# Kernel optimization log

Hardware: AMD Instinct MI355X
Metric: run time of the kernel (lower is better)

The kernel has to match this reference:

```python
import jax, jax.numpy as jnp
import numpy as np
from jax.scipy.linalg import expm

B, S, D, E, K, NROT = 2, 2048, 1024, 8, 2, 3
EPS = 1e-5


def setup_inputs() -> dict:
    key = jax.random.key(0)
    ks = jax.random.split(key, 16)
    sc = 0.02
    x = jax.random.normal(ks[0], (B, S, D), jnp.float32)
    ln_gamma = 1.0 + sc * jax.random.normal(ks[1], (D,), jnp.float32)
    ln_beta = sc * jax.random.normal(ks[2], (D,), jnp.float32)
    abel_w = sc * jax.random.normal(ks[3], (D, D), jnp.float32)
    abel_b = sc * jax.random.normal(ks[4], (D,), jnp.float32)
    moe_gate_w = sc * jax.random.normal(ks[5], (D, E), jnp.float32)
    moe_gate_b = sc * jax.random.normal(ks[6], (E,), jnp.float32)
    ew1 = sc * jax.random.normal(ks[7], (E, D, 2 * D), jnp.float32)
    eb1 = sc * jax.random.normal(ks[8], (E, 2 * D), jnp.float32)
    ew2 = sc * jax.random.normal(ks[9], (E, 2 * D, D), jnp.float32)
    eb2 = sc * jax.random.normal(ks[10], (E, D), jnp.float32)
    g = sc * jax.random.normal(ks[11], (NROT, D, D), jnp.float32)
    gens = 0.5 * (g - jnp.swapaxes(g, -1, -2))  # skew-symmetric, as in reset_parameters
    gc_w = sc * jax.random.normal(ks[12], (2 * D, 1), jnp.float32)
    gc_b = sc * jax.random.normal(ks[13], (1,), jnp.float32)
    return dict(x=x, ln_gamma=ln_gamma, ln_beta=ln_beta, abel_w=abel_w, abel_b=abel_b,
                moe_gate_w=moe_gate_w, moe_gate_b=moe_gate_b, ew1=ew1, eb1=eb1,
                ew2=ew2, eb2=eb2, gens=gens, gc_w=gc_w, gc_b=gc_b)


def _gelu(x):
    return jax.nn.gelu(x, approximate=False)  # torch nn.GELU default = exact erf


def _forward(x, ln_gamma, ln_beta, abel_w, abel_b, moe_gate_w, moe_gate_b,
             ew1, eb1, ew2, eb2, gens, gc_w, gc_b):
    residual = x
    # LayerNorm
    mu = jnp.mean(x, axis=-1, keepdims=True)
    var = jnp.mean((x - mu) ** 2, axis=-1, keepdims=True)
    xn = (x - mu) * jax.lax.rsqrt(var + EPS) * ln_gamma + ln_beta
    # abel branch: Linear + GELU
    abel_out = _gelu(xn @ abel_w + abel_b)
    # MoE: dense all-experts compute, masked by top-k softmax weights
    logits = xn @ moe_gate_w + moe_gate_b                      # [B,S,E]
    topw, topi = jax.lax.top_k(logits, K)                      # [B,S,K]
    topw = jax.nn.softmax(topw, axis=-1)
    w_dense = jnp.sum(jax.nn.one_hot(topi, E, dtype=xn.dtype) * topw[..., None], axis=-2)  # [B,S,E]
    h = _gelu(jnp.einsum('bsd,edh->ebsh', xn, ew1) + eb1[:, None, None, :])  # [E,B,S,2D]
    eo = jnp.einsum('ebsh,ehd->ebsd', h, ew2) + eb2[:, None, None, :]        # [E,B,S,D]
    moe_out = jnp.einsum('ebsd,bse->bsd', eo, w_dense)
    # GeometricRotation: sequential matrix_exp rotations
    for i in range(NROT):
        moe_out = moe_out @ expm(gens[i])
    # gated residual mix
    combined = jnp.concatenate([abel_out, moe_out], axis=-1)
    gate = jax.nn.sigmoid(combined @ gc_w + gc_b)              # [B,S,1]
    mixed = abel_out * (1.0 - gate) + moe_out * gate
    return residual + mixed


def reference(x, ln_gamma, ln_beta, abel_w, abel_b, moe_gate_w, moe_gate_b,
              ew1, eb1, ew2, eb2, gens, gc_w, gc_b):
    return _forward(x, ln_gamma, ln_beta, abel_w, abel_b, moe_gate_w, moe_gate_b,
                    ew1, eb1, ew2, eb2, gens, gc_w, gc_b)
```

## Files before the change

kernel.cpp:

```cpp
#include <hip/hip_runtime.h>
#include <hip/hip_bf16.h>
#include <cstdint>
#include <cstddef>

#define DD   1024
#define DD2  2048
#define EE   8
#define NTOK 4096
#define CAPR 9216

typedef __bf16 bf16_t;
typedef __bf16 bf16x8 __attribute__((ext_vector_type(8)));
typedef __bf16 bf16x4 __attribute__((ext_vector_type(4)));
typedef float  f32x4v __attribute__((ext_vector_type(4)));

__device__ __forceinline__ float gelu_f(float v){
  return 0.5f*v*(1.0f + erff(v*0.70710678118654752440f));
}

__device__ __forceinline__ void gload_lds16(const void* g, void* l){
  __builtin_amdgcn_global_load_lds(
    (const __attribute__((address_space(1))) unsigned int*)(uintptr_t)g,
    (__attribute__((address_space(3))) unsigned int*)(uintptr_t)l,
    16, 0, 0);
}

enum { EPI_GELU_F32=0, EPI_GELU_BF16=1, EPI_BIAS_BF16=2, EPI_SCALE_BF16=3,
       EPI_ADDV_BF16=4, EPI_BF16=5, EPI_F32=6 };

template<int BM,int BN,int EPI,bool DYN>
__global__ __launch_bounds__(256)
void gemm_bt(const bf16_t* __restrict__ A, const bf16_t* __restrict__ Bt,
             const bf16_t* __restrict__ Bt2,
             const int N, const int K,
             const long sAz, const long sBz, const long sOz, const int zsplit,
             const int* __restrict__ cnt, const int* __restrict__ offp,
             const float* __restrict__ bias, const long sBias,
             const float alpha, const float alpha2,
             const bf16_t* __restrict__ addv,
             float* __restrict__ outF, bf16_t* __restrict__ outB)
{
  constexpr int BK = 64;
  constexpr int WM = BM/2, WN = BN/2;
  constexpr int FM = WM/16, FN = WN/16;
  constexpr int IA = BM/32, IB = BN/32;
  __shared__ alignas(16) bf16_t sA[BM*BK];
  __shared__ alignas(16) bf16_t sB[BN*BK];

  const int z = blockIdx.z;
  int zz = z; const bf16_t* Bp = Bt; float al = alpha;
  if (z >= zsplit) { zz = z - zsplit; Bp = Bt2; al = alpha2; }

  float*  oF = outF;
  bf16_t* oB = outB;
  if constexpr (DYN) {
    const int Me = cnt[z];
    if ((int)(blockIdx.y * BM) >= Me) return;
    const long ro = offp[z];
    A  += ro * (long)K;
    oB += ro * (long)N;
  } else {
    A += (size_t)zz * sAz;
    if (oF) oF += (size_t)z * sOz;
    if (oB) oB += (size_t)z * sOz;
  }
  Bp += (size_t)zz * sBz;
  const float*  bp = bias ? bias + (size_t)z * sBias : nullptr;
  const bf16_t* vp = addv ? addv + (size_t)z * sOz   : nullptr;

  const int tid = threadIdx.x;
  const int wid = tid >> 6, lid = tid & 63;
  const int wr = wid >> 1, wc = wid & 1;
  const int brow = blockIdx.y * BM, bcol = blockIdx.x * BN;
  const int sr = lid >> 3, sq = lid & 7;
  const int fr = lid & 15, fq = lid >> 4;

  f32x4v acc[FM][FN] = {};

  for (int kt = 0; kt < K; kt += BK) {
    #pragma unroll
    for (int i = 0; i < IA; i++) {
      const int ii = wid*IA + i;
      const int r  = ii*8 + sr;
      const int q  = sq ^ (r & 7);
      gload_lds16((const char*)A + ((size_t)(brow + r)*K + kt)*2 + q*16,
                  (char*)sA + ii*1024);
    }
    #pragma unroll
    for (int i = 0; i < IB; i++) {
      const int ii = wid*IB + i;
      const int r  = ii*8 + sr;
      const int q  = sq ^ (r & 7);
      gload_lds16((const char*)Bp + ((size_t)(bcol + r)*K + kt)*2 + q*16,
                  (char*)sB + ii*1024);
    }
    __syncthreads();

    #pragma unroll
    for (int kk = 0; kk < 2; kk++) {
      bf16x8 af[FM], bb[FN];
      #pragma unroll
      for (int mi = 0; mi < FM; mi++) {
        const int r = wr*WM + mi*16 + fr;
        const int q = (kk*4 + fq) ^ (r & 7);
        af[mi] = *(const bf16x8*)((const char*)sA + r*128 + q*16);
      }
      #pragma unroll
      for (int ni = 0; ni < FN; ni++) {
        const int r = wc*WN + ni*16 + fr;
        const int q = (kk*4 + fq) ^ (r & 7);
        bb[ni] = *(const bf16x8*)((const char*)sB + r*128 + q*16);
      }
      #pragma unroll
      for (int mi = 0; mi < FM; mi++)
        #pragma unroll
        for (int ni = 0; ni < FN; ni++)
          acc[mi][ni] = __builtin_amdgcn_mfma_f32_16x16x32_bf16(
              af[mi], bb[ni], acc[mi][ni], 0, 0, 0);
    }
    __syncthreads();
  }

  #pragma unroll
  for (int mi = 0; mi < FM; mi++) {
    #pragma unroll
    for (int ni = 0; ni < FN; ni++) {
      const int rg0 = brow + wr*WM + mi*16 + fq*4;
      const int cg  = bcol + wc*WN + ni*16 + fr;
      #pragma unroll
      for (int i = 0; i < 4; i++) {
        const int rg = rg0 + i;
        float v = acc[mi][ni][i];
        if constexpr (EPI == EPI_GELU_F32) {
          v += bp[cg];
          oF[(size_t)rg*N + cg] = gelu_f(v);
        } else if constexpr (EPI == EPI_GELU_BF16) {
          v += bp[cg];
          oB[(size_t)rg*N + cg] = (bf16_t)gelu_f(v);
        } else if constexpr (EPI == EPI_BIAS_BF16) {
          v += bp[cg];
          oB[(size_t)rg*N + cg] = (bf16_t)v;
        } else if constexpr (EPI == EPI_SCALE_BF16) {
          oB[(size_t)rg*N + cg] = (bf16_t)(v * al);
        } else if constexpr (EPI == EPI_ADDV_BF16) {
          oB[(size_t)rg*N + cg] = (bf16_t)(v + (float)vp[(size_t)rg*N + cg]);
        } else if constexpr (EPI == EPI_BF16) {
          oB[(size_t)rg*N + cg] = (bf16_t)v;
        } else {
          oF[(size_t)rg*N + cg] = v;
        }
      }
    }
  }
}

__global__ __launch_bounds__(256)
void tcvt_kernel(const float* __restrict__ src, bf16_t* __restrict__ dst, int R, int C){
  __shared__ float tile[32][33];
  const size_t bo = (size_t)blockIdx.z * R * C;
  const int c0 = blockIdx.x*32, r0 = blockIdx.y*32;
  #pragma unroll
  for (int i = 0; i < 4; i++) {
    const int r = r0 + threadIdx.y + i*8;
    tile[threadIdx.y + i*8][threadIdx.x] = src[bo + (size_t)r*C + c0 + threadIdx.x];
  }
  __syncthreads();
  #pragma unroll
  for (int i = 0; i < 4; i++) {
    const int c = c0 + threadIdx.y + i*8;
    dst[bo + (size_t)c*R + r0 + threadIdx.x] = (bf16_t)tile[threadIdx.x][threadIdx.y + i*8];
  }
}

__global__ __launch_bounds__(256)
void tb16_kernel(const bf16_t* __restrict__ Ut, bf16_t* __restrict__ Tb){
  __shared__ bf16_t tile[32][33];
  const bf16_t* src = Ut + (size_t)(1 - blockIdx.z) * DD * DD;
  bf16_t*       dst = Tb + (size_t)blockIdx.z * DD * DD;
  const int c0 = blockIdx.x*32, r0 = blockIdx.y*32;
  #pragma unroll
  for (int i = 0; i < 4; i++)
    tile[threadIdx.y + i*8][threadIdx.x] = src[(size_t)(r0 + threadIdx.y + i*8)*DD + c0 + threadIdx.x];
  __syncthreads();
  #pragma unroll
  for (int i = 0; i < 4; i++)
    dst[(size_t)(c0 + threadIdx.y + i*8)*DD + r0 + threadIdx.x] = tile[threadIdx.x][threadIdx.y + i*8];
}

__global__ __launch_bounds__(256)
void cvt_kernel(const float* __restrict__ in, bf16_t* __restrict__ o, long n, float scale){
  const long i = ((long)blockIdx.x*256 + threadIdx.x)*4;
  if (i >= n) return;
  const float4 v = *(const float4*)(in + i);
  bf16x4 b; b[0]=(bf16_t)(v.x*scale); b[1]=(bf16_t)(v.y*scale);
  b[2]=(bf16_t)(v.z*scale); b[3]=(bf16_t)(v.w*scale);
  *(bf16x4*)(o + i) = b;
}

__global__ __launch_bounds__(256)
void vw_kernel(const bf16_t* __restrict__ Hn, const bf16_t* __restrict__ H2,
               const bf16_t* __restrict__ H3, bf16_t* __restrict__ Vb,
               bf16_t* __restrict__ Wtb){
  const long i0 = ((long)blockIdx.x*256 + threadIdx.x)*4;
  const long rc = i0 % (long)(DD*DD);
  const int r = (int)(rc / DD), c0 = (int)(rc % DD);
  const bf16x4 h  = *(const bf16x4*)(Hn + i0);
  const bf16x4 h2 = *(const bf16x4*)(H2 + i0);
  const bf16x4 h3 = *(const bf16x4*)(H3 + i0);
  bf16x4 v, w;
  #pragma unroll
  for (int j = 0; j < 4; j++) {
    const float d  = (r == c0 + j) ? 1.0f : 0.0f;
    const float fh = (float)h[j], f2 = (float)h2[j], f3 = (float)h3[j];
    v[j] = (bf16_t)(d + fh + f2*0.5f + f3*(1.0f/6.0f));
    w[j] = (bf16_t)(d*(1.0f/24.0f) - fh*(1.0f/120.0f) + f2*(1.0f/720.0f) - f3*(1.0f/5040.0f));
  }
  *(bf16x4*)(Vb  + i0) = v;
  *(bf16x4*)(Wtb + i0) = w;
}

__global__ __launch_bounds__(256)
void ln_gate_kernel(const float* __restrict__ x, const float* __restrict__ gamma,
                    const float* __restrict__ beta, const float* __restrict__ gw,
                    const float* __restrict__ gb,
                    bf16_t* __restrict__ xnb, int2* __restrict__ ids,
                    float2* __restrict__ wts)
{
  const int t = blockIdx.x, tid = threadIdx.x, j0 = tid*4;
  const int wid = tid >> 6, lid = tid & 63;
  const float4 v = *(const float4*)(x + (size_t)t*DD + j0);
  float s  = v.x + v.y + v.z + v.w;
  float ss = v.x*v.x + v.y*v.y + v.z*v.z + v.w*v.w;
  #pragma unroll
  for (int off = 32; off; off >>= 1) { s += __shfl_down(s, off); ss += __shfl_down(ss, off); }
  __shared__ float redS[4], redQ[4], mv[2];
  if (lid == 0) { redS[wid] = s; redQ[wid] = ss; }
  __syncthreads();
  if (tid == 0) {
    const float S1 = redS[0]+redS[1]+redS[2]+redS[3];
    const float S2 = redQ[0]+redQ[1]+redQ[2]+redQ[3];
    const float mu  = S1 * (1.0f/DD);
    const float var = S2 * (1.0f/DD) - mu*mu;
    mv[0] = mu; mv[1] = rsqrtf(var + 1e-5f);
  }
  __syncthreads();
  const float mu = mv[0], rstd = mv[1];
  const float4 g = *(const float4*)(gamma + j0);
  const float4 b = *(const float4*)(beta  + j0);
  float xn[4];
  xn[0] = (v.x-mu)*rstd*g.x + b.x;
  xn[1] = (v.y-mu)*rstd*g.y + b.y;
  xn[2] = (v.z-mu)*rstd*g.z + b.z;
  xn[3] = (v.w-mu)*rstd*g.w + b.w;
  bf16x4 ov; ov[0]=(bf16_t)xn[0]; ov[1]=(bf16_t)xn[1]; ov[2]=(bf16_t)xn[2]; ov[3]=(bf16_t)xn[3];
  *(bf16x4*)(xnb + (size_t)t*DD + j0) = ov;

  float p[8] = {0,0,0,0,0,0,0,0};
  #pragma unroll
  for (int i = 0; i < 4; i++) {
    const float4 a0 = *(const float4*)(gw + (size_t)(j0+i)*EE);
    const float4 a1 = *(const float4*)(gw + (size_t)(j0+i)*EE + 4);
    const float xv = xn[i];
    p[0]+=xv*a0.x; p[1]+=xv*a0.y; p[2]+=xv*a0.z; p[3]+=xv*a0.w;
    p[4]+=xv*a1.x; p[5]+=xv*a1.y; p[6]+=xv*a1.z; p[7]+=xv*a1.w;
  }
  #pragma unroll
  for (int off = 32; off; off >>= 1) {
    #pragma unroll
    for (int e = 0; e < 8; e++) p[e] += __shfl_down(p[e], off);
  }
  __shared__ float pr[32];
  if (lid == 0) {
    #pragma unroll
    for (int e = 0; e < 8; e++) pr[wid*8 + e] = p[e];
  }
  __syncthreads();
  if (tid == 0) {
    float l[8];
    #pragma unroll
    for (int e = 0; e < 8; e++) l[e] = pr[e] + pr[8+e] + pr[16+e] + pr[24+e] + gb[e];
    int i1 = 0; float m1 = l[0];
    #pragma unroll
    for (int e = 1; e < 8; e++) if (l[e] > m1) { m1 = l[e]; i1 = e; }
    int i2 = 0; float m2 = -1e30f;
    #pragma unroll
    for (int e = 0; e < 8; e++) if (e != i1 && l[e] > m2) { m2 = l[e]; i2 = e; }
    const float wa = 1.0f/(1.0f + expf(m2 - m1));
    ids[t] = make_int2(i1, i2);
    wts[t] = make_float2(wa, 1.0f - wa);
  }
}

__global__ __launch_bounds__(256)
void route_kernel(const int2* __restrict__ ids, int* __restrict__ slotA,
                  int* __restrict__ slotB, int* __restrict__ cnt)
{
  const int e = blockIdx.x;
  const int tid = threadIdx.x;
  const int wid = tid >> 6, lid = tid & 63;
  __shared__ int wsum[4];
  int base = 0;
  const unsigned long long lt = (1ull << lid) - 1ull;
  for (int c0 = 0; c0 < NTOK; c0 += 256) {
    const int t = c0 + tid;
    const int2 id = ids[t];
    const bool fA = (id.x == e), fB = (id.y == e);
    const unsigned long long mA = __ballot(fA);
    const unsigned long long mB = __ballot(fB);
    const int cA = __popcll(mA), cB = __popcll(mB);
    const int pA = __popcll(mA & lt), pB = __popcll(mB & lt);
    if (lid == 0) wsum[wid] = cA + cB;
    __syncthreads();
    int wbase = 0;
    #pragma unroll
    for (int w = 0; w < 4; w++) if (w < wid) wbase += wsum[w];
    const int tot = wsum[0] + wsum[1] + wsum[2] + wsum[3];
    if (fA) slotA[t] = base + wbase + pA;
    if (fB) slotB[t] = base + wbase + cA + pB;
    base += tot;
    __syncthreads();
  }
  if (tid == 0) cnt[e] = base;
}

__global__ void offs_kernel(const int* __restrict__ cnt, int* __restrict__ off){
  if (threadIdx.x == 0) {
    int a = 0;
    for (int e = 0; e < EE; e++) { off[e] = a; a += (cnt[e] + 127) & ~127; }
  }
}

__global__ __launch_bounds__(256)
void gather_kernel(const bf16_t* __restrict__ xnb, const int2* __restrict__ ids,
                   const int* __restrict__ slotA, const int* __restrict__ slotB,
                   const int* __restrict__ off, bf16_t* __restrict__ Xg){
  const int t = blockIdx.x, j = threadIdx.x*4;
  const int2 id = ids[t];
  const bf16x4 v = *(const bf16x4*)(xnb + (size_t)t*DD + j);
  *(bf16x4*)(Xg + (size_t)(off[id.x] + slotA[t])*DD + j) = v;
  *(bf16x4*)(Xg + (size_t)(off[id.y] + slotB[t])*DD + j) = v;
}

__global__ __launch_bounds__(256)
void combine_kernel(const bf16_t* __restrict__ Yg, const int2* __restrict__ ids,
                    const int* __restrict__ slotA, const int* __restrict__ slotB,
                    const int* __restrict__ off, const float2* __restrict__ wts,
                    bf16_t* __restrict__ Xa){
  const int t = blockIdx.x, j = threadIdx.x*4;
  const int2 id = ids[t];
  const float2 w = wts[t];
  const bf16x4 a = *(const bf16x4*)(Yg + (size_t)(off[id.x] + slotA[t])*DD + j);
  const bf16x4 b = *(const bf16x4*)(Yg + (size_t)(off[id.y] + slotB[t])*DD + j);
  bf16x4 o;
  #pragma unroll
  for (int i = 0; i < 4; i++) o[i] = (bf16_t)(w.x*(float)a[i] + w.y*(float)b[i]);
  *(bf16x4*)(Xa + (size_t)t*DD + j) = o;
}

__global__ __launch_bounds__(256)
void mix_kernel(const float* __restrict__ x, const float* __restrict__ abel,
                const float* __restrict__ rot, const float* __restrict__ gcw,
                const float* __restrict__ gcb, float* __restrict__ out)
{
  const int t = blockIdx.x, tid = threadIdx.x, j0 = tid*4;
  const int wid = tid >> 6, lid = tid & 63;
  const float4 a  = *(const float4*)(abel + (size_t)t*DD + j0);
  const float4 r  = *(const float4*)(rot  + (size_t)t*DD + j0);
  const float4 ga = *(const float4*)(gcw + j0);
  const float4 gr = *(const float4*)(gcw + DD + j0);
  float p = a.x*ga.x + a.y*ga.y + a.z*ga.z + a.w*ga.w
          + r.x*gr.x + r.y*gr.y + r.z*gr.z + r.w*gr.w;
  #pragma unroll
  for (int off = 32; off; off >>= 1) p += __shfl_down(p, off);
  __shared__ float red[4];
  __shared__ float gsh;
  if (lid == 0) red[wid] = p;
  __syncthreads();
  if (tid == 0) {
    const float P = red[0] + red[1] + red[2] + red[3] + gcb[0];
    gsh = 1.0f/(1.0f + expf(-P));
  }
  __syncthreads();
  const float gate = gsh, g1 = 1.0f - gate;
  const float4 xv = *(const float4*)(x + (size_t)t*DD + j0);
  float4 o;
  o.x = xv.x + a.x*g1 + r.x*gate;
  o.y = xv.y + a.y*g1 + r.y*gate;
  o.z = xv.z + a.z*g1 + r.z*gate;
  o.w = xv.w + a.w*g1 + r.w*gate;
  *(float4*)(out + (size_t)t*DD + j0) = o;
}

extern "C" void kernel_launch(void* const* d_in, const int* in_sizes, int n_in,
                              void* d_out, int out_size, void* d_ws, size_t ws_size,
                              hipStream_t stream)
{
  (void)in_sizes; (void)n_in; (void)out_size; (void)ws_size;
  const float* x      = (const float*)d_in[0];
  const float* ln_g   = (const float*)d_in[1];
  const float* ln_b   = (const float*)d_in[2];
  const float* abel_w = (const float*)d_in[3];
  const float* abel_b = (const float*)d_in[4];
  const float* gate_w = (const float*)d_in[5];
  const float* gate_b = (const float*)d_in[6];
  const float* ew1    = (const float*)d_in[7];
  const float* eb1    = (const float*)d_in[8];
  const float* ew2    = (const float*)d_in[9];
  const float* eb2    = (const float*)d_in[10];
  const float* gens   = (const float*)d_in[11];
  const float* gc_w   = (const float*)d_in[12];
  const float* gc_b   = (const float*)d_in[13];
  float* out = (float*)d_out;

  char* wsp = (char*)d_ws;
  auto alloc = [&](size_t bytes) -> char* {
    char* p = wsp; wsp += (bytes + 255) & ~(size_t)255; return p;
  };
  const size_t MB = 1u<<20;
  bf16_t* xnb   = (bf16_t*)alloc((size_t)NTOK*DD*2);
  int2*   ids   = (int2*)  alloc((size_t)NTOK*8);
  float2* wts   = (float2*)alloc((size_t)NTOK*8);
  int*    slotA = (int*)   alloc((size_t)NTOK*4);
  int*    slotB = (int*)   alloc((size_t)NTOK*4);
  int*    cnt   = (int*)   alloc(64);
  int*    off   = (int*)   alloc(64);
  bf16_t* abel_wT = (bf16_t*)alloc((size_t)DD*DD*2);
  char*   UN      = alloc(64*MB);
  bf16_t* ew1T  = (bf16_t*)UN;
  bf16_t* ew2T  = (bf16_t*)(UN + 32*MB);
  bf16_t* Hn    = (bf16_t*)alloc((size_t)3*DD*DD*2);
  float*  abelo = (float*) alloc((size_t)NTOK*DD*4);
  bf16_t* Xg    = (bf16_t*)alloc((size_t)CAPR*DD*2);
  bf16_t* Hg    = (bf16_t*)alloc((size_t)CAPR*DD2*2);
  bf16_t* Xa    = (bf16_t*)alloc((size_t)NTOK*DD*2);
  bf16_t* Yg    = Xg;
  float*  rot   = (float*)Hg;
  bf16_t* H2  = (bf16_t*)(UN + 0*MB);
  bf16_t* H34 = (bf16_t*)(UN + 6*MB);
  bf16_t* Vb  = (bf16_t*)(UN + 18*MB);
  bf16_t* Wtb = (bf16_t*)(UN + 24*MB);
  bf16_t* Ut  = (bf16_t*)(UN + 30*MB);
  bf16_t* Tb  = (bf16_t*)(UN + 36*MB);
  bf16_t* Pb  = (bf16_t*)(UN + 40*MB);
  bf16_t* Rt  = (bf16_t*)(UN + 42*MB);
  const long D2 = (long)DD*DD;

  const dim3 tb(32, 8, 1);
  tcvt_kernel<<<dim3(DD/32,  DD/32, 1),  tb, 0, stream>>>(abel_w, abel_wT, DD,  DD);
  tcvt_kernel<<<dim3(DD2/32, DD/32, EE), tb, 0, stream>>>(ew1,    ew1T,    DD,  DD2);
  tcvt_kernel<<<dim3(DD/32,  DD2/32,EE), tb, 0, stream>>>(ew2,    ew2T,    DD2, DD);
  cvt_kernel<<<dim3(3*DD*DD/1024,1,1), 256, 0, stream>>>(gens, Hn, (long)3*DD*DD, -1.0f);

  ln_gate_kernel<<<dim3(NTOK,1,1), 256, 0, stream>>>(x, ln_g, ln_b, gate_w, gate_b,
                                                     xnb, ids, wts);
  route_kernel<<<dim3(EE,1,1), 256, 0, stream>>>(ids, slotA, slotB, cnt);
  offs_kernel<<<dim3(1,1,1), 64, 0, stream>>>(cnt, off);
  gather_kernel<<<dim3(NTOK,1,1), 256, 0, stream>>>(xnb, ids, slotA, slotB, off, Xg);

  gemm_bt<128,128,EPI_GELU_BF16,true><<<dim3(DD2/128, NTOK/128, EE), 256, 0, stream>>>(
      Xg, ew1T, nullptr, DD2, DD, 0, (long)DD2*DD, 0, 1<<30, cnt, off,
      eb1, DD2, 1.0f, 0.0f, nullptr, nullptr, Hg);
  gemm_bt<128,64,EPI_BIAS_BF16,true><<<dim3(DD/64, NTOK/128, EE), 256, 0, stream>>>(
      Hg, ew2T, nullptr, DD, DD2, 0, (long)DD*DD2, 0, 1<<30, cnt, off,
      eb2, DD, 1.0f, 0.0f, nullptr, nullptr, Yg);
  combine_kernel<<<dim3(NTOK,1,1), 256, 0, stream>>>(Yg, ids, slotA, slotB, off, wts, Xa);

  gemm_bt<128,64,EPI_GELU_F32,false><<<dim3(DD/64, NTOK/128, 1), 256, 0, stream>>>(
      xnb, abel_wT, nullptr, DD, DD, 0, 0, 0, 1<<30, nullptr, nullptr,
      abel_b, 0, 1.0f, 0.0f, nullptr, abelo, nullptr);

  gemm_bt<64,64,EPI_SCALE_BF16,false><<<dim3(16,16,3), 256, 0, stream>>>(
      Hn, Hn, nullptr, DD, DD, D2, D2, D2, 1<<30, nullptr, nullptr,
      nullptr, 0, -1.0f, 0.0f, nullptr, nullptr, H2);
  gemm_bt<64,64,EPI_SCALE_BF16,false><<<dim3(16,16,6), 256, 0, stream>>>(
      H2, Hn, H2, DD, DD, D2, D2, D2, 3, nullptr, nullptr,
      nullptr, 0, -1.0f, 1.0f, nullptr, nullptr, H34);
  vw_kernel<<<dim3(3*DD*DD/1024,1,1), 256, 0, stream>>>(Hn, H2, H34, Vb, Wtb);
  gemm_bt<64,64,EPI_ADDV_BF16,false><<<dim3(16,16,3), 256, 0, stream>>>(
      H34 + 3*D2, Wtb, nullptr, DD, DD, D2, D2, D2, 1<<30, nullptr, nullptr,
      nullptr, 0, 1.0f, 0.0f, Vb, nullptr, Ut);
  tb16_kernel<<<dim3(32,32,2), tb, 0, stream>>>(Ut, Tb);
  gemm_bt<64,64,EPI_BF16,false><<<dim3(16,16,1), 256, 0, stream>>>(
      Ut + 2*D2, Tb, nullptr, DD, DD, 0, 0, 0, 1<<30, nullptr, nullptr,
      nullptr, 0, 1.0f, 0.0f, nullptr, nullptr, Pb);
  gemm_bt<64,64,EPI_BF16,false><<<dim3(16,16,1), 256, 0, stream>>>(
      Pb, Tb + D2, nullptr, DD, DD, 0, 0, 0, 1<<30, nullptr, nullptr,
      nullptr, 0, 1.0f, 0.0f, nullptr, nullptr, Rt);
  gemm_bt<128,64,EPI_F32,false><<<dim3(DD/64, NTOK/128, 1), 256, 0, stream>>>(
      Xa, Rt, nullptr, DD, DD, 0, 0, 0, 1<<30, nullptr, nullptr,
      nullptr, 0, 1.0f, 0.0f, nullptr, rot, nullptr);

  mix_kernel<<<dim3(NTOK,1,1), 256, 0, stream>>>(x, abelo, rot, gc_w, gc_b, out);
}
```

Measured before the change: 388.2 us.

## Flatten GEMM grids with XCD-aware block remapping and larger tiles

Replaces the 3D GEMM grids with a 1D grid whose block index is remapped so that consecutive logical tiles land on the same XCD (blockIdx mod 8). MoE expert GEMMs map each expert to one XCD, and dense GEMMs split contiguous tile ranges per XCD, aiming for better L2 reuse of shared A/B panels. Expert down-projection and the matrix-exponential GEMMs also move to 128-row tiles. The larger tiles mean fewer workgroups on the 1024x1024 GEMMs, and pinning each expert to one XCD can cause load imbalance when expert counts are skewed.

```diff
diff --git a/kernel.cpp b/kernel.cpp
--- a/kernel.cpp
+++ b/kernel.cpp
@@ -32,7 +32,7 @@
 __global__ __launch_bounds__(256)
 void gemm_bt(const bf16_t* __restrict__ A, const bf16_t* __restrict__ Bt,
              const bf16_t* __restrict__ Bt2,
-             const int N, const int K,
+             const int N, const int K, const int gx, const int gy, const int gz,
              const long sAz, const long sBz, const long sOz, const int zsplit,
              const int* __restrict__ cnt, const int* __restrict__ offp,
              const float* __restrict__ bias, const long sBias,
@@ -47,15 +47,28 @@
   __shared__ alignas(16) bf16_t sA[BM*BK];
   __shared__ alignas(16) bf16_t sB[BN*BK];
 
-  const int z = blockIdx.z;
+  int bx, by, bz;
+  if constexpr (DYN) {
+    const int e = blockIdx.x & 7;
+    const int i = blockIdx.x >> 3;
+    bz = e; by = i / gx; bx = i - by*gx;
+    if (by * BM >= cnt[e]) return;
+  } else {
+    const int nwg = gx * gy * gz;
+    const int q = nwg >> 3, r = nwg & 7;
+    const int k = blockIdx.x & 7, i = blockIdx.x >> 3;
+    if (i >= q + (k < r ? 1 : 0)) return;
+    const int l = k * q + (k < r ? k : r) + i;
+    bx = l % gx; const int t2 = l / gx; by = t2 % gy; bz = t2 / gy;
+  }
+
+  const int z = bz;
   int zz = z; const bf16_t* Bp = Bt; float al = alpha;
   if (z >= zsplit) { zz = z - zsplit; Bp = Bt2; al = alpha2; }
 
   float*  oF = outF;
   bf16_t* oB = outB;
   if constexpr (DYN) {
-    const int Me = cnt[z];
-    if ((int)(blockIdx.y * BM) >= Me) return;
     const long ro = offp[z];
     A  += ro * (long)K;
     oB += ro * (long)N;
@@ -71,7 +84,7 @@
   const int tid = threadIdx.x;
   const int wid = tid >> 6, lid = tid & 63;
   const int wr = wid >> 1, wc = wid & 1;
-  const int brow = blockIdx.y * BM, bcol = blockIdx.x * BN;
+  const int brow = by * BM, bcol = bx * BN;
   const int sr = lid >> 3, sq = lid & 7;
   const int fr = lid & 15, fq = lid >> 4;
 
@@ -445,6 +458,10 @@
   bf16_t* Rt  = (bf16_t*)(UN + 42*MB);
   const long D2 = (long)DD*DD;
 
+  auto gflat = [](int gx, int gy, int gz) {
+    const int nwg = gx*gy*gz; return 8 * ((nwg + 7) / 8);
+  };
+
   const dim3 tb(32, 8, 1);
   tcvt_kernel<<<dim3(DD/32,  DD/32, 1),  tb, 0, stream>>>(abel_w, abel_wT, DD,  DD);
   tcvt_kernel<<<dim3(DD2/32, DD/32, EE), tb, 0, stream>>>(ew1,    ew1T,    DD,  DD2);
@@ -457,37 +474,37 @@
   offs_kernel<<<dim3(1,1,1), 64, 0, stream>>>(cnt, off);
   gather_kernel<<<dim3(NTOK,1,1), 256, 0, stream>>>(xnb, ids, slotA, slotB, off, Xg);
 
-  gemm_bt<128,128,EPI_GELU_BF16,true><<<dim3(DD2/128, NTOK/128, EE), 256, 0, stream>>>(
-      Xg, ew1T, nullptr, DD2, DD, 0, (long)DD2*DD, 0, 1<<30, cnt, off,
-      eb1, DD2, 1.0f, 0.0f, nullptr, nullptr, Hg);
-  gemm_bt<128,64,EPI_BIAS_BF16,true><<<dim3(DD/64, NTOK/128, EE), 256, 0, stream>>>(
-      Hg, ew2T, nullptr, DD, DD2, 0, (long)DD*DD2, 0, 1<<30, cnt, off,
-      eb2, DD, 1.0f, 0.0f, nullptr, nullptr, Yg);
+  gemm_bt<128,128,EPI_GELU_BF16,true><<<dim3(8*(DD2/128)*(NTOK/128),1,1), 256, 0, stream>>>(
+      Xg, ew1T, nullptr, DD2, DD, DD2/128, NTOK/128, EE, 0, (long)DD2*DD, 0, 1<<30,
+      cnt, off, eb1, DD2, 1.0f, 0.0f, nullptr, nullptr, Hg);
+  gemm_bt<128,128,EPI_BIAS_BF16,true><<<dim3(8*(DD/128)*(NTOK/128),1,1), 256, 0, stream>>>(
+      Hg, ew2T, nullptr, DD, DD2, DD/128, NTOK/128, EE, 0, (long)DD*DD2, 0, 1<<30,
+      cnt, off, eb2, DD, 1.0f, 0.0f, nullptr, nullptr, Yg);
   combine_kernel<<<dim3(NTOK,1,1), 256, 0, stream>>>(Yg, ids, slotA, slotB, off, wts, Xa);
 
-  gemm_bt<128,64,EPI_GELU_F32,false><<<dim3(DD/64, NTOK/128, 1), 256, 0, stream>>>(
-      xnb, abel_wT, nullptr, DD, DD, 0, 0, 0, 1<<30, nullptr, nullptr,
+  gemm_bt<128,64,EPI_GELU_F32,false><<<dim3(gflat(16,32,1),1,1), 256, 0, stream>>>(
+      xnb, abel_wT, nullptr, DD, DD, 16, 32, 1, 0, 0, 0, 1<<30, nullptr, nullptr,
       abel_b, 0, 1.0f, 0.0f, nullptr, abelo, nullptr);
 
-  gemm_bt<64,64,EPI_SCALE_BF16,false><<<dim3(16,16,3), 256, 0, stream>>>(
-      Hn, Hn, nullptr, DD, DD, D2, D2, D2, 1<<30, nullptr, nullptr,
+  gemm_bt<128,64,EPI_SCALE_BF16,false><<<dim3(gflat(16,8,3),1,1), 256, 0, stream>>>(
+      Hn, Hn, nullptr, DD, DD, 16, 8, 3, D2, D2, D2, 1<<30, nullptr, nullptr,
       nullptr, 0, -1.0f, 0.0f, nullptr, nullptr, H2);
-  gemm_bt<64,64,EPI_SCALE_BF16,false><<<dim3(16,16,6), 256, 0, stream>>>(
-      H2, Hn, H2, DD, DD, D2, D2, D2, 3, nullptr, nullptr,
+  gemm_bt<128,64,EPI_SCALE_BF16,false><<<dim3(gflat(16,8,6),1,1), 256, 0, stream>>>(
+      H2, Hn, H2, DD, DD, 16, 8, 6, D2, D2, D2, 3, nullptr, nullptr,
       nullptr, 0, -1.0f, 1.0f, nullptr, nullptr, H34);
   vw_kernel<<<dim3(3*DD*DD/1024,1,1), 256, 0, stream>>>(Hn, H2, H34, Vb, Wtb);
-  gemm_bt<64,64,EPI_ADDV_BF16,false><<<dim3(16,16,3), 256, 0, stream>>>(
-      H34 + 3*D2, Wtb, nullptr, DD, DD, D2, D2, D2, 1<<30, nullptr, nullptr,
+  gemm_bt<128,64,EPI_ADDV_BF16,false><<<dim3(gflat(16,8,3),1,1), 256, 0, stream>>>(
+      H34 + 3*D2, Wtb, nullptr, DD, DD, 16, 8, 3, D2, D2, D2, 1<<30, nullptr, nullptr,
       nullptr, 0, 1.0f, 0.0f, Vb, nullptr, Ut);
   tb16_kernel<<<dim3(32,32,2), tb, 0, stream>>>(Ut, Tb);
-  gemm_bt<64,64,EPI_BF16,false><<<dim3(16,16,1), 256, 0, stream>>>(
-      Ut + 2*D2, Tb, nullptr, DD, DD, 0, 0, 0, 1<<30, nullptr, nullptr,
+  gemm_bt<128,64,EPI_BF16,false><<<dim3(gflat(16,8,1),1,1), 256, 0, stream>>>(
+      Ut + 2*D2, Tb, nullptr, DD, DD, 16, 8, 1, 0, 0, 0, 1<<30, nullptr, nullptr,
       nullptr, 0, 1.0f, 0.0f, nullptr, nullptr, Pb);
-  gemm_bt<64,64,EPI_BF16,false><<<dim3(16,16,1), 256, 0, stream>>>(
-      Pb, Tb + D2, nullptr, DD, DD, 0, 0, 0, 1<<30, nullptr, nullptr,
+  gemm_bt<128,64,EPI_BF16,false><<<dim3(gflat(16,8,1),1,1), 256, 0, stream>>>(
+      Pb, Tb + D2, nullptr, DD, DD, 16, 8, 1, 0, 0, 0, 1<<30, nullptr, nullptr,
       nullptr, 0, 1.0f, 0.0f, nullptr, nullptr, Rt);
-  gemm_bt<128,64,EPI_F32,false><<<dim3(DD/64, NTOK/128, 1), 256, 0, stream>>>(
-      Xa, Rt, nullptr, DD, DD, 0, 0, 0, 1<<30, nullptr, nullptr,
+  gemm_bt<128,64,EPI_F32,false><<<dim3(gflat(16,32,1),1,1), 256, 0, stream>>>(
+      Xa, Rt, nullptr, DD, DD, 16, 32, 1, 0, 0, 0, 1<<30, nullptr, nullptr,
       nullptr, 0, 1.0f, 0.0f, nullptr, rot, nullptr);
 
   mix_kernel<<<dim3(NTOK,1,1), 256, 0, stream>>>(x, abelo, rot, gc_w, gc_b, out);
```

Result: faster. 377.6 us (-2.7%).
